# Performance work log

Measured on AMD Instinct MI355X. Metric: run time of the kernel, lower is better.

## Reference

```python
import jax, jax.numpy as jnp
import numpy as np

B, XL, YL, D = 16, 2048, 2048, 1024

def setup_inputs() -> dict:
    key = jax.random.key(0)
    kx, ky, km, kw = jax.random.split(key, 4)
    x = jax.random.normal(kx, (B, XL, D), dtype=jnp.float32)
    y = jax.random.normal(ky, (B, YL, D), dtype=jnp.float32)
    # True == padding position (masked with -inf in the torch module)
    y_mask = jax.random.randint(km, (B, YL), 0, 2).astype(bool)
    # shared projection Linear(embed_dim, embed_dim); scale ~ 1/sqrt(D)
    W = jax.random.normal(kw, (D, D), dtype=jnp.float32) * (1.0 / np.sqrt(D))
    b = jnp.zeros((D,), dtype=jnp.float32)
    return {"x": x, "y": y, "y_mask": y_mask, "W": W, "b": b}

def reference(x, y, y_mask, W, b):
    # shared ReLU(Linear) projection applied to both x and y
    x_proj = jax.nn.relu(jnp.einsum('bxd,ed->bxe', x, W) + b)   # (B, XL, D)
    y_proj = jax.nn.relu(jnp.einsum('byd,ed->bye', y, W) + b)   # (B, YL, D)
    scores = jnp.einsum('bxd,byd->bxy', x_proj, y_proj)          # (B, XL, YL)
    scores = jnp.where(y_mask[:, None, :], -jnp.inf, scores)
    weights = jax.nn.softmax(scores, axis=2)
    contexts = jnp.einsum('bxy,byd->bxd', weights, y)            # (B, XL, D)
    return contexts
```

## Files before the change

### kernel.cpp

```cpp
#include <hip/hip_runtime.h>
#include <math.h>
#include <stdint.h>


typedef __attribute__((ext_vector_type(8))) _Float16 f16x8;
typedef __attribute__((ext_vector_type(4))) float f32x4;

__device__ __forceinline__ ushort h2u(_Float16 h) { return __builtin_bit_cast(ushort, h); }

__device__ __forceinline__ void ld16(const ushort* g, ushort* l) {
    __builtin_amdgcn_global_load_lds(
        (__attribute__((address_space(1))) void*)(g),
        (__attribute__((address_space(3))) void*)(l), 16, 0, 0);
}

template<int EPI, int MODE>
__global__ __launch_bounds__(256, 2) void gemmw(
    const ushort* __restrict__ A, size_t zsA,
    const ushort* __restrict__ B, size_t zsB,
    const float* __restrict__ bias, const int* __restrict__ nyBuf,
    float* __restrict__ Cf, ushort* __restrict__ Chi, size_t zsC,
    int sdA, int sdB, int N, int T)
{
    __shared__ char ldsb[49152];

    const int gx = gridDim.x, gxy = gx * gridDim.y;
    const int total = gxy * gridDim.z;
    int hsw = blockIdx.z * gxy + blockIdx.y * gx + blockIdx.x;
    hsw = (hsw & 7) * (total >> 3) + (hsw >> 3);
    const int z = hsw / gxy;
    const int rem = hsw - z * gxy;
    const int by = rem / gx;
    const int bx = rem - by * gx;

    int NY = 0, NYPAD = 0;
    if constexpr (MODE != 0) { NY = nyBuf[2 * z]; NYPAD = nyBuf[2 * z + 1]; }
    const int m0 = by * 128, n0 = bx * 256;
    if constexpr (MODE == 1) { if (m0 >= 2048 && m0 - 2048 >= NYPAD) return; }
    if constexpr (MODE == 2) { if (n0 >= NYPAD) return; }
    if constexpr (MODE == 3) { T = NYPAD >> 6; }

    const int tid = threadIdx.x;
    const int lane = tid & 63;
    const int wv = tid >> 6;
    const int wm = (wv >> 1) * 64;
    const int wn = (wv & 1) * 128;

    const int pl  = tid >> 3;
    const int ss  = (tid & 7) ^ (pl & 7);
    const int sr0 = 2 * pl + (ss >> 2);
    const int ske = (ss & 3) * 8;
    const int tb  = tid * 16;

    const ushort* gA0 = A + (size_t)z * zsA + (size_t)(m0 + sr0) * sdA + ske;
    const ushort* gA1 = gA0 + (size_t)64 * sdA;
    const ushort* gB0 = B + (size_t)z * zsB + (size_t)(n0 + sr0) * sdB + ske;
    const ushort* gB1 = gB0 + (size_t)64 * sdB;
    const ushort* gB2 = gB0 + (size_t)128 * sdB;
    const ushort* gB3 = gB0 + (size_t)192 * sdB;

    const int fr = lane & 15, fq = lane >> 4;
    const int sl = (((fr & 1) << 2) | fq) ^ ((fr >> 1) & 7);
    const int aoff = wm * 64 + (fr >> 1) * 128 + sl * 16;
    const int boff = 16384 + wn * 64 + (fr >> 1) * 128 + sl * 16;

    f32x4 acc[4][8];
    #pragma unroll
    for (int i = 0; i < 4; ++i)
        #pragma unroll
        for (int j = 0; j < 8; ++j)
            acc[i][j] = (f32x4){0.f, 0.f, 0.f, 0.f};

    for (int t = 0; t < T; ++t) {
        ld16(gA0,      (ushort*)(ldsb + tb));
        ld16(gA1,      (ushort*)(ldsb + 4096 + tb));
        ld16(gA0 + 32, (ushort*)(ldsb + 8192 + tb));
        ld16(gA1 + 32, (ushort*)(ldsb + 12288 + tb));
        ld16(gB0,      (ushort*)(ldsb + 16384 + tb));
        ld16(gB1,      (ushort*)(ldsb + 20480 + tb));
        ld16(gB2,      (ushort*)(ldsb + 24576 + tb));
        ld16(gB3,      (ushort*)(ldsb + 28672 + tb));
        ld16(gB0 + 32, (ushort*)(ldsb + 32768 + tb));
        ld16(gB1 + 32, (ushort*)(ldsb + 36864 + tb));
        ld16(gB2 + 32, (ushort*)(ldsb + 40960 + tb));
        ld16(gB3 + 32, (ushort*)(ldsb + 45056 + tb));
        gA0 += 64; gA1 += 64; gB0 += 64; gB1 += 64; gB2 += 64; gB3 += 64;
        __syncthreads();

        #pragma unroll
        for (int kk = 0; kk < 2; ++kk) {
            const char* pa = ldsb + kk * 8192 + aoff;
            const char* pb = ldsb + kk * 16384 + boff;
            f16x8 a[4], b[8];
            #pragma unroll
            for (int i = 0; i < 4; ++i) a[i] = *(const f16x8*)(pa + i * 1024);
            #pragma unroll
            for (int j = 0; j < 8; ++j) b[j] = *(const f16x8*)(pb + j * 1024);
            #pragma unroll
            for (int i = 0; i < 4; ++i)
                #pragma unroll
                for (int j = 0; j < 8; ++j)
                    acc[i][j] = __builtin_amdgcn_mfma_f32_16x16x32_f16(a[i], b[j], acc[i][j], 0, 0, 0);
        }
        __syncthreads();
    }

    #pragma unroll
    for (int j = 0; j < 8; ++j) {
        const int col = n0 + wn + j * 16 + fr;
        float bb = 0.f;
        if constexpr (EPI == 1) bb = bias[col];
        #pragma unroll
        for (int i = 0; i < 4; ++i) {
            const int row = m0 + wm + i * 16 + fq * 4;
            #pragma unroll
            for (int r = 0; r < 4; ++r) {
                const float v = acc[i][j][r];
                const size_t o = (size_t)z * zsC + (size_t)(row + r) * N + col;
                if constexpr (EPI == 0) {
                    Cf[o] = v;
                } else if constexpr (EPI == 1) {
                    Chi[o] = h2u((_Float16)fmaxf(v + bb, 0.f));
                } else {
                    Cf[o] = (col >= NY) ? -INFINITY : v;
                }
            }
        }
    }
}

__global__ __launch_bounds__(256) void build_idx(const int* __restrict__ mask,
    int* __restrict__ idx, int* __restrict__ nyBuf)
{
    const int z = blockIdx.x;
    const int* mb = mask + (size_t)z * 2048;
    __shared__ int part[256];
    const int tid = threadIdx.x;
    int keep[8]; int c = 0;
    #pragma unroll
    for (int k = 0; k < 8; ++k) { keep[k] = (mb[tid * 8 + k] == 0); c += keep[k]; }
    part[tid] = c;
    for (int off = 1; off < 256; off <<= 1) {
        __syncthreads();
        const int v = (tid >= off) ? part[tid - off] : 0;
        __syncthreads();
        part[tid] += v;
    }
    __syncthreads();
    int pos = part[tid] - c;
    #pragma unroll
    for (int k = 0; k < 8; ++k)
        if (keep[k]) idx[(size_t)z * 2048 + (pos++)] = tid * 8 + k;
    if (tid == 255) {
        const int ny = part[255];
        int nyp = (ny + 127) & ~127;
        if (nyp < 256) nyp = 256;
        nyBuf[2 * z] = ny;
        nyBuf[2 * z + 1] = nyp;
    }
}

__global__ __launch_bounds__(256) void cvt_f16(const float* __restrict__ in,
    ushort* __restrict__ o, size_t sIn4, size_t sOut)
{
    const size_t z = blockIdx.z;
    const int i = blockIdx.x * 256 + threadIdx.x;
    const float4 v = reinterpret_cast<const float4*>(in)[z * sIn4 + i];
    ushort4 h;
    h.x = h2u((_Float16)v.x); h.y = h2u((_Float16)v.y);
    h.z = h2u((_Float16)v.z); h.w = h2u((_Float16)v.w);
    reinterpret_cast<ushort4*>(o + z * sOut)[i] = h;
}

__global__ __launch_bounds__(256) void gather_y(const float* __restrict__ y,
    const int* __restrict__ idx, const int* __restrict__ nyBuf,
    ushort* __restrict__ rH, ushort* __restrict__ tT,
    size_t sIn, size_t sR, size_t sT)
{
    __shared__ float tile[32][33];
    const size_t z = blockIdx.z;
    const int NY = nyBuf[2 * z], NYPAD = nyBuf[2 * z + 1];
    const int r0 = blockIdx.y * 32;
    if (r0 >= NYPAD) return;
    const int c0 = blockIdx.x * 32;
    const float* yb = y + z * sIn;
    const int* idxb = idx + z * 2048;
    const int tx = threadIdx.x & 31, ty = threadIdx.x >> 5;
    #pragma unroll
    for (int k = 0; k < 4; ++k) {
        const int i = r0 + ty + k * 8;
        float v = 0.f;
        if (i < NY) v = yb[(size_t)idxb[i] * 1024 + c0 + tx];
        tile[ty + k * 8][tx] = v;
        rH[z * sR + (size_t)i * 1024 + c0 + tx] = h2u((_Float16)v);
    }
    __syncthreads();
    #pragma unroll
    for (int k = 0; k < 4; ++k) {
        const int c = c0 + ty + k * 8;
        tT[z * sT + (size_t)c * 2048 + r0 + tx] = h2u((_Float16)tile[tx][ty + k * 8]);
    }
}

__global__ __launch_bounds__(256) void softmax_f16(const float* __restrict__ S,
    ushort* __restrict__ Wout, const int* __restrict__ nyBuf, size_t sS, size_t sW)
{
    const size_t row = blockIdx.x;
    const size_t b = row >> 11, r = row & 2047;
    const int nf4 = nyBuf[2 * b + 1] >> 2;
    const float4* p4 = reinterpret_cast<const float4*>(S + b * sS + r * 2048);
    ushort4* q4 = reinterpret_cast<ushort4*>(Wout + b * sW + r * 2048);
    const int tid = threadIdx.x;

    const float4 NEG = {-INFINITY, -INFINITY, -INFINITY, -INFINITY};
    float4 v0 = (tid < nf4) ? p4[tid] : NEG;
    float4 v1 = (tid + 256 < nf4) ? p4[tid + 256] : NEG;
    float m = fmaxf(fmaxf(fmaxf(v0.x, v0.y), fmaxf(v0.z, v0.w)),
                    fmaxf(fmaxf(v1.x, v1.y), fmaxf(v1.z, v1.w)));
    #pragma unroll
    for (int off = 32; off >= 1; off >>= 1)
        m = fmaxf(m, __shfl_xor(m, off));

    __shared__ float redm[4], reds[4];
    if ((tid & 63) == 0) redm[tid >> 6] = m;
    __syncthreads();
    m = fmaxf(fmaxf(redm[0], redm[1]), fmaxf(redm[2], redm[3]));

    float e[8];
    e[0] = __expf(v0.x - m); e[1] = __expf(v0.y - m);
    e[2] = __expf(v0.z - m); e[3] = __expf(v0.w - m);
    e[4] = __expf(v1.x - m); e[5] = __expf(v1.y - m);
    e[6] = __expf(v1.z - m); e[7] = __expf(v1.w - m);
    float s = ((e[0] + e[1]) + (e[2] + e[3])) + ((e[4] + e[5]) + (e[6] + e[7]));
    #pragma unroll
    for (int off = 32; off >= 1; off >>= 1)
        s += __shfl_xor(s, off);
    if ((tid & 63) == 0) reds[tid >> 6] = s;
    __syncthreads();
    s = reds[0] + reds[1] + reds[2] + reds[3];

    const float inv = 1.f / s;
    ushort4 o0, o1;
    o0.x = h2u((_Float16)(e[0] * inv)); o0.y = h2u((_Float16)(e[1] * inv));
    o0.z = h2u((_Float16)(e[2] * inv)); o0.w = h2u((_Float16)(e[3] * inv));
    o1.x = h2u((_Float16)(e[4] * inv)); o1.y = h2u((_Float16)(e[5] * inv));
    o1.z = h2u((_Float16)(e[6] * inv)); o1.w = h2u((_Float16)(e[7] * inv));
    if (tid < nf4) q4[tid] = o0;
    if (tid + 256 < nf4) q4[tid + 256] = o1;
}

extern "C" void kernel_launch(void* const* d_in, const int* in_sizes, int n_in,
                              void* d_out, int out_size, void* d_ws, size_t ws_size,
                              hipStream_t stream)
{
    const float* x    = (const float*)d_in[0];
    const float* y    = (const float*)d_in[1];
    const int* ymask  = (const int*)d_in[2];
    const float* W    = (const float*)d_in[3];
    const float* bias = (const float*)d_in[4];
    float* out = (float*)d_out;

    const size_t BD = 2097152;

    const size_t perBatch = 29360128ull;
    int G = 16;
    while (G > 1 && 4194304ull + (size_t)G * perBatch > ws_size) G >>= 1;

    uint8_t* wsb = (uint8_t*)d_ws;
    ushort* W16  = (ushort*)wsb;
    int* idxBuf  = (int*)(wsb + 2097152);
    int* nyBuf   = (int*)(wsb + 2097152 + 131072);
    uint8_t* r1  = wsb + 4194304;
    uint8_t* r2  = r1 + (size_t)G * 16777216;
    uint8_t* r3  = r2 + (size_t)G * 8388608;

    ushort* xyHi = (ushort*)r1;
    float*  sc   = (float*)r1;
    ushort* pHi  = (ushort*)r2;
    ushort* yT   = (ushort*)r3;

    cvt_f16<<<dim3(1024, 1, 1), dim3(256), 0, stream>>>(W, W16, 0, 0);
    build_idx<<<dim3(16), dim3(256), 0, stream>>>(ymask, idxBuf, nyBuf);

    for (int bs = 0; bs < 16; bs += G) {
        const float* xg = x + (size_t)bs * BD;
        const float* yg = y + (size_t)bs * BD;
        const int* nyB  = nyBuf + 2 * bs;

        cvt_f16<<<dim3(2048, 1, G), dim3(256), 0, stream>>>(
            xg, xyHi, BD / 4, 8388608);
        gather_y<<<dim3(32, 64, G), dim3(256), 0, stream>>>(
            yg, idxBuf + (size_t)bs * 2048, nyB,
            xyHi + BD, yT, BD, 8388608, BD);

        gemmw<1, 1><<<dim3(4, 32, G), dim3(256), 0, stream>>>(
            xyHi, 8388608, W16, 0,
            bias, nyB,
            nullptr, pHi, 4194304, 1024, 1024, 1024, 16);

        gemmw<2, 2><<<dim3(8, 16, G), dim3(256), 0, stream>>>(
            pHi, 4194304, pHi + BD, 4194304,
            nullptr, nyB,
            sc, nullptr, 4194304, 1024, 1024, 2048, 16);

        softmax_f16<<<dim3(G * 2048), dim3(256), 0, stream>>>(
            sc, pHi, nyB, 4194304, 4194304);

        gemmw<0, 3><<<dim3(4, 16, G), dim3(256), 0, stream>>>(
            pHi, 4194304, yT, 2097152,
            nullptr, nyB,
            out + (size_t)bs * BD, nullptr, BD, 2048, 2048, 1024, 16);
    }
}
```

Measured before the change: 515.2 us.

## Triple-buffer GEMM K tiles with async LDS prefetch two stages ahead

Restructures the shared GEMM main loop from a synchronous load-then-compute over 64-wide K tiles into a three-stage ring of 32-wide K tiles. Global-to-LDS loads run two tiles ahead, and explicit vmcnt waits plus raw barriers replace __syncthreads. This is meant to hide global memory latency behind MFMA work. In exchange it raises LDS use to 72KB per block, which may limit occupancy, and halves the compute per barrier pair.

```diff
diff --git a/kernel.cpp b/kernel.cpp
--- a/kernel.cpp
+++ b/kernel.cpp
@@ -13,6 +13,9 @@
         (__attribute__((address_space(1))) void*)(g),
         (__attribute__((address_space(3))) void*)(l), 16, 0, 0);
 }
+
+#define BAR()   { __builtin_amdgcn_s_barrier(); asm volatile("" ::: "memory"); }
+#define VMW(N)  asm volatile("s_waitcnt vmcnt(" #N ")" ::: "memory");
 
 template<int EPI, int MODE>
 __global__ __launch_bounds__(256, 2) void gemmw(
@@ -22,7 +25,7 @@
     float* __restrict__ Cf, ushort* __restrict__ Chi, size_t zsC,
     int sdA, int sdB, int N, int T)
 {
-    __shared__ char ldsb[49152];
+    __shared__ char ldsb[73728];
 
     const int gx = gridDim.x, gxy = gx * gridDim.y;
     const int total = gxy * gridDim.z;
@@ -38,7 +41,7 @@
     const int m0 = by * 128, n0 = bx * 256;
     if constexpr (MODE == 1) { if (m0 >= 2048 && m0 - 2048 >= NYPAD) return; }
     if constexpr (MODE == 2) { if (n0 >= NYPAD) return; }
-    if constexpr (MODE == 3) { T = NYPAD >> 6; }
+    if constexpr (MODE == 3) { T = NYPAD >> 5; }
 
     const int tid = threadIdx.x;
     const int lane = tid & 63;
@@ -62,7 +65,7 @@
     const int fr = lane & 15, fq = lane >> 4;
     const int sl = (((fr & 1) << 2) | fq) ^ ((fr >> 1) & 7);
     const int aoff = wm * 64 + (fr >> 1) * 128 + sl * 16;
-    const int boff = 16384 + wn * 64 + (fr >> 1) * 128 + sl * 16;
+    const int boff = 8192 + wn * 64 + (fr >> 1) * 128 + sl * 16;
 
     f32x4 acc[4][8];
     #pragma unroll
@@ -71,26 +74,34 @@
         for (int j = 0; j < 8; ++j)
             acc[i][j] = (f32x4){0.f, 0.f, 0.f, 0.f};
 
+    auto stage = [&](int ko, int buf) {
+        char* d = ldsb + buf * 24576;
+        ld16(gA0 + ko, (ushort*)(d + tb));
+        ld16(gA1 + ko, (ushort*)(d + 4096 + tb));
+        ld16(gB0 + ko, (ushort*)(d + 8192 + tb));
+        ld16(gB1 + ko, (ushort*)(d + 12288 + tb));
+        ld16(gB2 + ko, (ushort*)(d + 16384 + tb));
+        ld16(gB3 + ko, (ushort*)(d + 20480 + tb));
+    };
+
+    stage(0, 0);
+    stage(32, 1);
+
+    int buf = 0;
     for (int t = 0; t < T; ++t) {
-        ld16(gA0,      (ushort*)(ldsb + tb));
-        ld16(gA1,      (ushort*)(ldsb + 4096 + tb));
-        ld16(gA0 + 32, (ushort*)(ldsb + 8192 + tb));
-        ld16(gA1 + 32, (ushort*)(ldsb + 12288 + tb));
-        ld16(gB0,      (ushort*)(ldsb + 16384 + tb));
-        ld16(gB1,      (ushort*)(ldsb + 20480 + tb));
-        ld16(gB2,      (ushort*)(ldsb + 24576 + tb));
-        ld16(gB3,      (ushort*)(ldsb + 28672 + tb));
-        ld16(gB0 + 32, (ushort*)(ldsb + 32768 + tb));
-        ld16(gB1 + 32, (ushort*)(ldsb + 36864 + tb));
-        ld16(gB2 + 32, (ushort*)(ldsb + 40960 + tb));
-        ld16(gB3 + 32, (ushort*)(ldsb + 45056 + tb));
-        gA0 += 64; gA1 += 64; gB0 += 64; gB1 += 64; gB2 += 64; gB3 += 64;
-        __syncthreads();
-
-        #pragma unroll
-        for (int kk = 0; kk < 2; ++kk) {
-            const char* pa = ldsb + kk * 8192 + aoff;
-            const char* pb = ldsb + kk * 16384 + boff;
+        if (t + 2 < T) {
+            stage(64, buf == 0 ? 2 : (buf - 1));
+            VMW(12);
+        } else if (t + 1 < T) {
+            VMW(6);
+        } else {
+            VMW(0);
+        }
+        BAR();
+
+        {
+            const char* pa = ldsb + buf * 24576 + aoff;
+            const char* pb = ldsb + buf * 24576 + boff;
             f16x8 a[4], b[8];
             #pragma unroll
             for (int i = 0; i < 4; ++i) a[i] = *(const f16x8*)(pa + i * 1024);
@@ -102,7 +113,10 @@
                 for (int j = 0; j < 8; ++j)
                     acc[i][j] = __builtin_amdgcn_mfma_f32_16x16x32_f16(a[i], b[j], acc[i][j], 0, 0, 0);
         }
-        __syncthreads();
+        BAR();
+
+        gA0 += 32; gA1 += 32; gB0 += 32; gB1 += 32; gB2 += 32; gB3 += 32;
+        buf = (buf == 2) ? 0 : (buf + 1);
     }
 
     #pragma unroll
@@ -296,12 +310,12 @@
         gemmw<1, 1><<<dim3(4, 32, G), dim3(256), 0, stream>>>(
             xyHi, 8388608, W16, 0,
             bias, nyB,
-            nullptr, pHi, 4194304, 1024, 1024, 1024, 16);
+            nullptr, pHi, 4194304, 1024, 1024, 1024, 32);
 
         gemmw<2, 2><<<dim3(8, 16, G), dim3(256), 0, stream>>>(
             pHi, 4194304, pHi + BD, 4194304,
             nullptr, nyB,
-            sc, nullptr, 4194304, 1024, 1024, 2048, 16);
+            sc, nullptr, 4194304, 1024, 1024, 2048, 32);
 
         softmax_f16<<<dim3(G * 2048), dim3(256), 0, stream>>>(
             sc, pHi, nyB, 4194304, 4194304);
@@ -309,6 +323,6 @@
         gemmw<0, 3><<<dim3(4, 16, G), dim3(256), 0, stream>>>(
             pHi, 4194304, yT, 2097152,
             nullptr, nyB,
-            out + (size_t)bs * BD, nullptr, BD, 2048, 2048, 1024, 16);
-    }
-}
+            out + (size_t)bs * BD, nullptr, BD, 2048, 2048, 1024, 32);
+    }
+}
```

New measurement: 499.6 us. 3.0% less time.
